# Optimization experiments

Hardware: AMD Instinct MI355X
Metric: run time of the kernel (lower is better)

## Reference

```python
import math
import jax, jax.numpy as jnp
import numpy as np

B, S, H, NH = 4, 2048, 1024, 16
HD = H // NH  # 64


def _rope_cos_sin(seq_len, dim, base=10000.0):
    # freqs[j] = base^(-2j/dim), angles = outer(t, freqs)
    inv = 1.0 / (base ** (jnp.arange(0, dim, 2, dtype=jnp.float32) / dim))
    t = jnp.arange(seq_len, dtype=jnp.float32)
    ang = jnp.outer(t, inv)  # (S, dim//2)
    return jnp.cos(ang), jnp.sin(ang)


def _apply_rope(x, cos, sin):
    # x: (B, S, NH, HD); pairs are (x[2i], x[2i+1]) per torch view_as_complex on reshape(..., -1, 2)
    xr = x.reshape(*x.shape[:-1], HD // 2, 2)
    x0, x1 = xr[..., 0], xr[..., 1]
    c = cos[None, :, None, :]  # (1, S, 1, HD//2)
    s = sin[None, :, None, :]
    o0 = x0 * c - x1 * s
    o1 = x0 * s + x1 * c
    return jnp.stack([o0, o1], axis=-1).reshape(x.shape)


def setup_inputs() -> dict:
    key = jax.random.key(0)
    ks = jax.random.split(key, 5)
    scale = 1.0 / math.sqrt(H)
    return {
        "x": jax.random.normal(ks[0], (B, S, H), dtype=jnp.float32),
        "wq": jax.random.normal(ks[1], (H, H), dtype=jnp.float32) * scale,
        "wk": jax.random.normal(ks[2], (H, H), dtype=jnp.float32) * scale,
        "wv": jax.random.normal(ks[3], (H, H), dtype=jnp.float32) * scale,
        "wo": jax.random.normal(ks[4], (H, H), dtype=jnp.float32) * scale,
        "attention_mask": jnp.ones((B, S), dtype=jnp.int32),
    }


def reference(x, wq, wk, wv, wo, attention_mask):
    # Linear(bias=False): y = x @ W.T with W shape (out, in)
    q = jnp.einsum('bsh,oh->bso', x, wq).reshape(B, S, NH, HD)
    k = jnp.einsum('bsh,oh->bso', x, wk).reshape(B, S, NH, HD)
    v = jnp.einsum('bsh,oh->bso', x, wv).reshape(B, S, NH, HD)
    cos, sin = _rope_cos_sin(S, HD)
    q = _apply_rope(q, cos, sin)
    k = _apply_rope(k, cos, sin)
    # scores: (B, NH, S, S)
    scores = jnp.einsum('bqhd,bkhd->bhqk', q, k) / math.sqrt(HD)
    mask = attention_mask[:, None, None, :]  # (B,1,1,S)
    scores = jnp.where(mask == 0, -jnp.inf, scores)
    attn = jax.nn.softmax(scores, axis=-1)
    # attn_dropout: eval mode / p=0 -> identity
    out = jnp.einsum('bhqk,bkhd->bqhd', attn, v).reshape(B, S, H)
    return jnp.einsum('bsh,oh->bso', out, wo)
```

## Files before the change

### kernel.cpp

```cpp
#include <hip/hip_runtime.h>
#include <hip/hip_bf16.h>

#define B_   4
#define S_   2048
#define H_   1024
#define NH_  16
#define HD_  64
#define M_   8192
#define K_   1024

using bf16x8 = __bf16 __attribute__((ext_vector_type(8)));
using f32x4  = float __attribute__((ext_vector_type(4)));
using f32x16 = float __attribute__((ext_vector_type(16)));

__device__ inline f32x4 mfma16(bf16x8 a, bf16x8 b, f32x4 c) {
    return __builtin_amdgcn_mfma_f32_16x16x32_bf16(a, b, c, 0, 0, 0);
}
__device__ inline f32x16 mfma32(bf16x8 a, bf16x8 b, f32x16 c) {
    return __builtin_amdgcn_mfma_f32_32x32x16_bf16(a, b, c, 0, 0, 0);
}

__device__ inline unsigned short f2bf(float f) {
    __hip_bfloat16 h = __float2bfloat16(f);
    return *reinterpret_cast<unsigned short*>(&h);
}

__device__ inline unsigned cvt_pk_bf16(float lo, float hi) {
    unsigned r;
    asm("v_cvt_pk_bf16_f32 %0, %1, %2" : "=v"(r) : "v"(lo), "v"(hi));
    return r;
}

__device__ inline void perm32swap(unsigned &a, unsigned &b) {
    asm("v_permlane32_swap_b32 %0, %1" : "+v"(a), "+v"(b));
}

__device__ inline void gload_lds16(const unsigned short* g, unsigned short* l) {
    __builtin_amdgcn_global_load_lds(
        (const __attribute__((address_space(1))) void*)g,
        (__attribute__((address_space(3))) void*)l, 16, 0, 0);
}

#define EXP2F(x) __builtin_amdgcn_exp2f(x)


__global__ __launch_bounds__(256) void prep_convert(
    const float* __restrict__ x,  const float* __restrict__ wq,
    const float* __restrict__ wk, const float* __restrict__ wv,
    const float* __restrict__ wo, unsigned short* __restrict__ ws)
{
    size_t u = (size_t)blockIdx.x * 256 + threadIdx.x;
    const float* src; unsigned short* dst; size_t off;
    if (u < 2097152)      { src = x;  dst = ws;            off = u * 4; }
    else if (u < 2359296) { src = wq; dst = ws + 8388608;  off = (u - 2097152) * 4; }
    else if (u < 2621440) { src = wk; dst = ws + 9437184;  off = (u - 2359296) * 4; }
    else if (u < 2883584) { src = wv; dst = ws + 10485760; off = (u - 2621440) * 4; }
    else                  { src = wo; dst = ws + 11534336; off = (u - 2883584) * 4; }
    float4 v = *reinterpret_cast<const float4*>(src + off);
    ushort4 o;
    o.x = f2bf(v.x); o.y = f2bf(v.y); o.z = f2bf(v.z); o.w = f2bf(v.w);
    *reinterpret_cast<ushort4*>(dst + off) = o;
}

__global__ __launch_bounds__(256) void rope_table(
    float2* __restrict__ ropeb, const int* __restrict__ mask,
    float* __restrict__ biasb)
{
    int idx = blockIdx.x * 256 + threadIdx.x;
    int pos = idx >> 5, i = idx & 31;
    float inv = expf(-(float)(2 * i) * (9.210340371976184f / 64.0f));
    float ang = (float)pos * inv;
    float2 cs; cs.x = cosf(ang); cs.y = sinf(ang);
    ropeb[idx] = cs;
    if (idx < B_ * S_)
        biasb[idx] = mask[idx] ? -12.0f : -__builtin_inff();
}

template<int MODE>
__global__ __launch_bounds__(256, 2) void gemm_main(
    const unsigned short* __restrict__ A,
    const unsigned short* __restrict__ W,
    unsigned short* __restrict__ qbuf, unsigned short* __restrict__ kbuf,
    unsigned short* __restrict__ vtb, float* __restrict__ fout,
    const float* __restrict__ ropeb)
{
    __shared__ alignas(16) unsigned short Al[2][128 * 64];
    __shared__ alignas(16) unsigned short Bl[2][128 * 64];

    const int t = threadIdx.x;
    const int l = t & 63;
    const int w = t >> 6;
    const int lane_r = l & 15, lane_g = l >> 4;
    const int bn = blockIdx.x, bm = blockIdx.y;
    const size_t rowbase = (size_t)bm * 128;
    const int colbase = bn * 128;
    const int wm = (w >> 1) * 64, wn = (w & 1) * 64;
    const int which = (MODE == 0) ? (colbase >> 10) : 3;
    const float scale = (which == 0) ? 0.18033688089184827f : 1.0f;

    const int glrow  = l >> 3;
    const int glslot = (l & 7) ^ glrow;
    const unsigned short* ga = A + (rowbase + w * 8 + glrow) * K_ + glslot * 8;
    const unsigned short* gb = W + (size_t)(colbase + w * 8 + glrow) * K_ + glslot * 8;

#define GLA(bi, kt, i) gload_lds16(ga + (size_t)(i) * 32 * K_ + (kt) * 64, \
                                   &Al[bi][((i) * 32 + w * 8) * 64]);
#define GLB(bi, kt, i) gload_lds16(gb + (size_t)(i) * 32 * K_ + (kt) * 64, \
                                   &Bl[bi][((i) * 32 + w * 8) * 64]);
#define RDA(mt, kk) { int rowa = wm + (mt) * 16 + lane_r;                      \
    af[mt][kk] = *reinterpret_cast<const bf16x8*>((const char*)Al[cur] +       \
        ((rowa * 128 + (kk) * 64 + lane_g * 16) ^ ((rowa & 7) << 4))); }
#define RDB(nt, kk) { int rowb = wn + (nt) * 16 + lane_r;                      \
    bfr[nt][kk] = *reinterpret_cast<const bf16x8*>((const char*)Bl[cur] +      \
        ((rowb * 128 + (kk) * 64 + lane_g * 16) ^ ((rowb & 7) << 4))); }
#define MM(mb, nb)                                                             \
    if (MODE == 0 && which <= 1) {                                             \
        _Pragma("unroll")                                                      \
        for (int a = (nb); a < (nb) + 2; a++)                                  \
            _Pragma("unroll")                                                  \
            for (int b2 = (mb); b2 < (mb) + 2; b2++) {                         \
                acc[a][b2] = mfma16(bfr[a][0], af[b2][0], acc[a][b2]);         \
                acc[a][b2] = mfma16(bfr[a][1], af[b2][1], acc[a][b2]);         \
            }                                                                  \
    } else {                                                                   \
        _Pragma("unroll")                                                      \
        for (int mt = (mb); mt < (mb) + 2; mt++)                               \
            _Pragma("unroll")                                                  \
            for (int nt = (nb); nt < (nb) + 2; nt++) {                         \
                acc[mt][nt] = mfma16(af[mt][0], bfr[nt][0], acc[mt][nt]);      \
                acc[mt][nt] = mfma16(af[mt][1], bfr[nt][1], acc[mt][nt]);      \
            }                                                                  \
    }
#define BARS __builtin_amdgcn_s_barrier();                                     \
             asm volatile("s_waitcnt lgkmcnt(0)" ::: "memory");                \
             __builtin_amdgcn_s_setprio(1);
#define BARE __builtin_amdgcn_s_setprio(0); __builtin_amdgcn_s_barrier();

    f32x4 zero4 = {0.f, 0.f, 0.f, 0.f};
    f32x4 acc[4][4];
#pragma unroll
    for (int a = 0; a < 4; a++)
#pragma unroll
        for (int b2 = 0; b2 < 4; b2++) acc[a][b2] = zero4;

    GLA(0, 0, 0) GLA(0, 0, 1) GLA(0, 0, 2) GLA(0, 0, 3)
    GLB(0, 0, 0) GLB(0, 0, 1) GLB(0, 0, 2) GLB(0, 0, 3)
    __syncthreads();

    for (int kt = 0; kt < 16; kt++) {
        const int cur = kt & 1, nxt = cur ^ 1;
        const bool pf = (kt < 15);
        bf16x8 af[4][2], bfr[4][2];
        RDA(0, 0) RDA(0, 1) RDA(1, 0) RDA(1, 1)
        RDB(0, 0) RDB(0, 1) RDB(1, 0) RDB(1, 1)
        if (pf) { GLA(nxt, kt + 1, 0) GLA(nxt, kt + 1, 1) GLA(nxt, kt + 1, 2) }
        BARS MM(0, 0) BARE
        RDB(2, 0) RDB(2, 1) RDB(3, 0) RDB(3, 1)
        if (pf) { GLA(nxt, kt + 1, 3) GLB(nxt, kt + 1, 0) GLB(nxt, kt + 1, 1) }
        BARS MM(0, 2) BARE
        RDA(2, 0) RDA(2, 1) RDA(3, 0) RDA(3, 1)
        if (pf) { GLB(nxt, kt + 1, 2) GLB(nxt, kt + 1, 3) }
        BARS MM(2, 2) BARE
        __builtin_amdgcn_s_setprio(1);
        MM(2, 0)
        __builtin_amdgcn_s_setprio(0);
        asm volatile("s_waitcnt vmcnt(0)" ::: "memory");
        __builtin_amdgcn_s_barrier();
    }
#undef GLA
#undef GLB
#undef RDA
#undef RDB
#undef MM
#undef BARS
#undef BARE

    if (MODE == 1) {
        float* out = fout;
#pragma unroll
        for (int mt = 0; mt < 4; mt++)
#pragma unroll
            for (int nt = 0; nt < 4; nt++)
#pragma unroll
                for (int i = 0; i < 4; i++) {
                    size_t r = rowbase + wm + mt * 16 + lane_g * 4 + i;
                    int n = colbase + wn + nt * 16 + lane_r;
                    out[r * 1024 + n] = acc[mt][nt][i];
                }
    } else if (which <= 1) {
        unsigned short* out = which ? kbuf : qbuf;
#pragma unroll
        for (int a = 0; a < 4; a++) {
            int nbase = (colbase & 1023) + wn + a * 16 + 4 * lane_g;
            int h = nbase >> 6, d0 = nbase & 63;
#pragma unroll
            for (int b2 = 0; b2 < 4; b2++) {
                size_t r = rowbase + wm + b2 * 16 + lane_r;
                int bb  = (int)(r >> 11);
                int pos = (int)(r & 2047);
                float4 cs = *reinterpret_cast<const float4*>(
                    ropeb + pos * 64 + d0);
                float a0 = acc[a][b2][0], a1 = acc[a][b2][1];
                float a2 = acc[a][b2][2], a3 = acc[a][b2][3];
                float o0 = (a0 * cs.x - a1 * cs.y) * scale;
                float o1 = (a0 * cs.y + a1 * cs.x) * scale;
                float o2 = (a2 * cs.z - a3 * cs.w) * scale;
                float o3 = (a2 * cs.w + a3 * cs.z) * scale;
                uint2 o;
                o.x = cvt_pk_bf16(o0, o1);
                o.y = cvt_pk_bf16(o2, o3);
                *reinterpret_cast<uint2*>(
                    out + (((size_t)(bb * NH_ + h)) * S_ + pos) * 64 + d0) = o;
            }
        }
    } else {
#pragma unroll
        for (int a = 0; a < 4; a++)
#pragma unroll
            for (int b2 = 0; b2 < 4; b2++) {
                size_t rr = rowbase + wm + a * 16 + lane_g * 4;
                int n = (colbase & 1023) + wn + b2 * 16 + lane_r;
                int bb  = (int)(rr >> 11);
                int pos = (int)(rr & 2047);
                int h = n >> 6, d = n & 63;
                ushort4 o;
                o.x = f2bf(acc[a][b2][0]); o.y = f2bf(acc[a][b2][1]);
                o.z = f2bf(acc[a][b2][2]); o.w = f2bf(acc[a][b2][3]);
                *reinterpret_cast<ushort4*>(
                    vtb + (((size_t)(bb * NH_ + h)) * 64 + d) * S_ + pos) = o;
            }
    }
}

__global__ __launch_bounds__(256, 2) void attn_fwd(
    const unsigned short* __restrict__ qb, const unsigned short* __restrict__ kb,
    const unsigned short* __restrict__ vt, const float* __restrict__ biasb,
    unsigned short* __restrict__ ao)
{
    __shared__ alignas(16) unsigned short Kl[2][64 * 64];
    __shared__ alignas(16) unsigned short Vl[2][64 * 64];

    const int bid = blockIdx.x;
    const int xcd = bid & 7, idx = bid >> 3;
    const int bh = xcd * 8 + (idx >> 3);
    const int qt = idx & 7;
    const int b = bh >> 4, h = bh & 15;

    const int t = threadIdx.x, l = t & 63, w = t >> 6;
    const int lr = l & 31;
    const int hi = l >> 5;
    const int row8 = lr & 7;

    const unsigned short* qp = qb + (size_t)bh * S_ * 64;
    const unsigned short* kp = kb + (size_t)bh * S_ * 64;
    const unsigned short* vp = vt + (size_t)bh * 64 * S_;
    const float* bp = biasb + (size_t)b * S_;

    bf16x8 qf[2][4];
#pragma unroll
    for (int qbk = 0; qbk < 2; qbk++) {
        int qrow = qt * 256 + w * 64 + qbk * 32 + lr;
#pragma unroll
        for (int ks = 0; ks < 4; ks++)
            qf[qbk][ks] = *reinterpret_cast<const bf16x8*>(
                qp + (size_t)qrow * 64 + ks * 16 + hi * 8);
    }

    f32x16 oacc[2][2];
#pragma unroll
    for (int qbk = 0; qbk < 2; qbk++)
#pragma unroll
        for (int r = 0; r < 16; r++) { oacc[qbk][0][r] = 0.f; oacc[qbk][1][r] = 0.f; }
    float lsum[2] = {0.f, 0.f};

    const int grr = l >> 3;
    const int gss = ((l & 7) ^ grr) * 8;

#define STAGE(bi, kt)                                                          \
    {                                                                          \
        _Pragma("unroll")                                                      \
        for (int c = 0; c < 2; c++) {                                          \
            int rbase = w * 16 + c * 8;                                        \
            gload_lds16(kp + (size_t)((kt) * 64 + rbase + grr) * 64 + gss,     \
                        &Kl[bi][rbase * 64]);                                  \
            gload_lds16(vp + (size_t)(rbase + grr) * S_ + (kt) * 64 + gss,     \
                        &Vl[bi][rbase * 64]);                                  \
        }                                                                      \
    }

    STAGE(0, 0)

    for (int kt = 0; kt < 32; kt++) {
        const int cur = kt & 1;
        __syncthreads();
        if (kt < 31) STAGE(cur ^ 1, kt + 1)

        f32x16 sacc[2][2];
#pragma unroll
        for (int T = 0; T < 2; T++) {
#pragma unroll
            for (int g = 0; g < 4; g++) {
                float4 bv = *reinterpret_cast<const float4*>(
                    bp + kt * 64 + T * 32 + g * 8 + hi * 4);
                sacc[0][T][g * 4 + 0] = bv.x; sacc[0][T][g * 4 + 1] = bv.y;
                sacc[0][T][g * 4 + 2] = bv.z; sacc[0][T][g * 4 + 3] = bv.w;
                sacc[1][T][g * 4 + 0] = bv.x; sacc[1][T][g * 4 + 1] = bv.y;
                sacc[1][T][g * 4 + 2] = bv.z; sacc[1][T][g * 4 + 3] = bv.w;
            }
        }

        __builtin_amdgcn_s_setprio(1);
#pragma unroll
        for (int T = 0; T < 2; T++) {
            int rowb = (32 * T + lr) * 128;
#pragma unroll
            for (int ks = 0; ks < 4; ks++) {
                bf16x8 kf = *reinterpret_cast<const bf16x8*>(
                    (const char*)Kl[cur] + rowb + (((2 * ks + hi) ^ row8) << 4));
                sacc[0][T] = mfma32(kf, qf[0][ks], sacc[0][T]);
                sacc[1][T] = mfma32(kf, qf[1][ks], sacc[1][T]);
            }
        }
        __builtin_amdgcn_s_setprio(0);

        bf16x8 pa[2][4];
#pragma unroll
        for (int qbk = 0; qbk < 2; qbk++) {
            unsigned u[2][8];
            float r0 = 0.f, r1 = 0.f, r2 = 0.f, r3 = 0.f;
#pragma unroll
            for (int T = 0; T < 2; T++) {
                float p[16];
#pragma unroll
                for (int r = 0; r < 16; r++) p[r] = EXP2F(sacc[qbk][T][r]);
#pragma unroll
                for (int r = 0; r < 16; r += 4) {
                    r0 += p[r]; r1 += p[r + 1]; r2 += p[r + 2]; r3 += p[r + 3];
                }
#pragma unroll
                for (int bq = 0; bq < 4; bq++) {
                    u[T][bq * 2 + 0] = cvt_pk_bf16(p[bq * 4 + 0], p[bq * 4 + 1]);
                    u[T][bq * 2 + 1] = cvt_pk_bf16(p[bq * 4 + 2], p[bq * 4 + 3]);
                }
            }
            lsum[qbk] += (r0 + r1) + (r2 + r3);
#pragma unroll
            for (int ks = 0; ks < 4; ks++) {
                int T = ks >> 1, e = ks & 1;
                unsigned a0 = u[T][4 * e + 0], b0 = u[T][4 * e + 2];
                unsigned a1 = u[T][4 * e + 1], b1 = u[T][4 * e + 3];
                perm32swap(a0, b0);
                perm32swap(a1, b1);
                unsigned q4[4] = {a0, a1, b0, b1};
                pa[qbk][ks] = *reinterpret_cast<const bf16x8*>(q4);
            }
        }

        __builtin_amdgcn_s_setprio(1);
#pragma unroll
        for (int dt = 0; dt < 2; dt++) {
            int rowb = (32 * dt + lr) * 128;
#pragma unroll
            for (int ks = 0; ks < 4; ks++) {
                bf16x8 vf = *reinterpret_cast<const bf16x8*>(
                    (const char*)Vl[cur] + rowb + (((2 * ks + hi) ^ row8) << 4));
                oacc[0][dt] = mfma32(vf, pa[0][ks], oacc[0][dt]);
                oacc[1][dt] = mfma32(vf, pa[1][ks], oacc[1][dt]);
            }
        }
        __builtin_amdgcn_s_setprio(0);
    }
#undef STAGE

#pragma unroll
    for (int qbk = 0; qbk < 2; qbk++) {
        float ls = lsum[qbk];
        ls += __shfl_xor(ls, 32);
        float rl = 1.0f / ls;
        size_t obase = ((size_t)(b * S_) + qt * 256 + w * 64 + qbk * 32 + lr) * 1024 + h * 64;
#pragma unroll
        for (int dt = 0; dt < 2; dt++)
#pragma unroll
            for (int g = 0; g < 4; g++) {
                uint2 o;
                o.x = cvt_pk_bf16(oacc[qbk][dt][g * 4 + 0] * rl, oacc[qbk][dt][g * 4 + 1] * rl);
                o.y = cvt_pk_bf16(oacc[qbk][dt][g * 4 + 2] * rl, oacc[qbk][dt][g * 4 + 3] * rl);
                *reinterpret_cast<uint2*>(ao + obase + 32 * dt + 8 * g + 4 * hi) = o;
            }
    }
}

extern "C" void kernel_launch(void* const* d_in, const int* in_sizes, int n_in,
                              void* d_out, int out_size, void* d_ws, size_t ws_size,
                              hipStream_t stream)
{
    const float* x  = (const float*)d_in[0];
    const float* wq = (const float*)d_in[1];
    const float* wk = (const float*)d_in[2];
    const float* wv = (const float*)d_in[3];
    const float* wo = (const float*)d_in[4];
    const int* mask = (const int*)d_in[5];

    unsigned short* ws   = (unsigned short*)d_ws;
    unsigned short* xb   = ws;
    unsigned short* wqkv = ws + 8388608;
    unsigned short* wob  = ws + 11534336;
    unsigned short* qbuf = ws + 12582912;
    unsigned short* kbuf = ws + 20971520;
    unsigned short* vtb  = ws + 29360128;
    float* ropeb = (float*)(ws + 37748736);
    float* biasb = (float*)(ws + 38010880);
    unsigned short* aob = xb;

    prep_convert<<<12288, 256, 0, stream>>>(x, wq, wk, wv, wo, ws);
    rope_table<<<256, 256, 0, stream>>>((float2*)ropeb, mask, biasb);

    gemm_main<0><<<dim3(24, 64), 256, 0, stream>>>(
        xb, wqkv, qbuf, kbuf, vtb, nullptr, ropeb);

    attn_fwd<<<512, 256, 0, stream>>>(qbuf, kbuf, vtb, biasb, aob);

    gemm_main<1><<<dim3(8, 64), 256, 0, stream>>>(
        aob, wob, nullptr, nullptr, nullptr, (float*)d_out, nullptr);
}
```

Measured before the change: 199.4 us.

## Use 256x256 tiles with 8 waves for fused QKV projection GEMM

Replaces the shared 128x128 GEMM template for the QKV projection with a dedicated kernel using 256x256 block tiles, 512 threads (8 waves, each computing 128x64), and a two-deep LDS pipeline that prefetches tile kt+2 while computing kt. The output projection becomes a separate simplified kernel. The goal is to raise arithmetic intensity and cut global/LDS reload traffic per MFMA. The cost is 128KB of LDS per block and 128 accumulator registers per thread, which lowers occupancy. The grid also shrinks to 384 blocks, which may underfill the CUs.

```diff
diff --git a/kernel.cpp b/kernel.cpp
--- a/kernel.cpp
+++ b/kernel.cpp
@@ -39,6 +39,11 @@
     __builtin_amdgcn_global_load_lds(
         (const __attribute__((address_space(1))) void*)g,
         (__attribute__((address_space(3))) void*)l, 16, 0, 0);
+}
+
+__device__ inline bf16x8 ldfrag(const unsigned short* base, int row, int kk, int lane_g) {
+    int off = (row * 128 + kk * 64 + lane_g * 16) ^ ((row & 7) << 4);
+    return *reinterpret_cast<const bf16x8*>((const char*)base + off);
 }
 
 #define EXP2F(x) __builtin_amdgcn_exp2f(x)
@@ -76,13 +81,177 @@
         biasb[idx] = mask[idx] ? -12.0f : -__builtin_inff();
 }
 
-template<int MODE>
-__global__ __launch_bounds__(256, 2) void gemm_main(
+__global__ __launch_bounds__(512, 2) void gemm_qkv256(
     const unsigned short* __restrict__ A,
     const unsigned short* __restrict__ W,
     unsigned short* __restrict__ qbuf, unsigned short* __restrict__ kbuf,
-    unsigned short* __restrict__ vtb, float* __restrict__ fout,
+    unsigned short* __restrict__ vtb,
     const float* __restrict__ ropeb)
+{
+    __shared__ alignas(16) unsigned short Al[2][256 * 64];
+    __shared__ alignas(16) unsigned short Bl[2][256 * 64];
+
+    const int t = threadIdx.x;
+    const int l = t & 63;
+    const int w = t >> 6;
+    const int lane_r = l & 15, lane_g = l >> 4;
+    const int bn = blockIdx.x, bm = blockIdx.y;
+    const size_t rowbase = (size_t)bm * 256;
+    const int colbase = bn * 256;
+    const int wr = w >> 2, wc = w & 3;
+    const int wm = wr * 128, wn = wc * 64;
+    const int which = bn >> 2;
+    const float scale = (which == 0) ? 0.18033688089184827f : 1.0f;
+
+    const int grr = l >> 3;
+    const int gss = ((l & 7) ^ grr) * 8;
+    const unsigned short* ga = A + (rowbase + w * 8 + grr) * K_ + gss;
+    const unsigned short* gb = W + (size_t)(colbase + w * 8 + grr) * K_ + gss;
+
+#define STAGE(bi, kt)                                                          \
+    { _Pragma("unroll")                                                        \
+      for (int c = 0; c < 4; c++) {                                            \
+          gload_lds16(ga + (size_t)(c * 64) * K_ + (kt) * 64,                  \
+                      &Al[bi][(c * 64 + w * 8) * 64]);                         \
+          gload_lds16(gb + (size_t)(c * 64) * K_ + (kt) * 64,                  \
+                      &Bl[bi][(c * 64 + w * 8) * 64]);                         \
+      } }
+
+#define BARF asm volatile("" ::: "memory");                                    \
+             __builtin_amdgcn_s_barrier();                                     \
+             asm volatile("" ::: "memory");
+#define PRIO1 __builtin_amdgcn_s_setprio(1);
+#define PRIO0 __builtin_amdgcn_s_setprio(0);
+
+#define QMM(MT0, NT0)                                                          \
+    if (which <= 1) {                                                          \
+        _Pragma("unroll")                                                      \
+        for (int mt = (MT0); mt < (MT0) + 4; mt++)                             \
+            _Pragma("unroll")                                                  \
+            for (int nt = (NT0); nt < (NT0) + 2; nt++) {                       \
+                acc[mt][nt] = mfma16(bfr[nt][0], af[mt - (MT0)][0], acc[mt][nt]); \
+                acc[mt][nt] = mfma16(bfr[nt][1], af[mt - (MT0)][1], acc[mt][nt]); \
+            }                                                                  \
+    } else {                                                                   \
+        _Pragma("unroll")                                                      \
+        for (int mt = (MT0); mt < (MT0) + 4; mt++)                             \
+            _Pragma("unroll")                                                  \
+            for (int nt = (NT0); nt < (NT0) + 2; nt++) {                       \
+                acc[mt][nt] = mfma16(af[mt - (MT0)][0], bfr[nt][0], acc[mt][nt]); \
+                acc[mt][nt] = mfma16(af[mt - (MT0)][1], bfr[nt][1], acc[mt][nt]); \
+            }                                                                  \
+    }
+
+#define TILE_PHASES(cur, kt, DO_ISSUE)                                         \
+    {                                                                          \
+        bf16x8 af[4][2], bfr[4][2];                                            \
+            \
+        _Pragma("unroll")                                                      \
+        for (int i = 0; i < 4; i++) {                                          \
+            int rowa = wm + i * 16 + lane_r;                                   \
+            af[i][0] = ldfrag(Al[cur], rowa, 0, lane_g);                       \
+            af[i][1] = ldfrag(Al[cur], rowa, 1, lane_g);                       \
+        }                                                                      \
+        _Pragma("unroll")                                                      \
+        for (int nt = 0; nt < 2; nt++) {                                       \
+            int rowb = wn + nt * 16 + lane_r;                                  \
+            bfr[nt][0] = ldfrag(Bl[cur], rowb, 0, lane_g);                     \
+            bfr[nt][1] = ldfrag(Bl[cur], rowb, 1, lane_g);                     \
+        }                                                                      \
+        BARF PRIO1 QMM(0, 0) PRIO0 BARF                                        \
+                              \
+        _Pragma("unroll")                                                      \
+        for (int nt = 2; nt < 4; nt++) {                                       \
+            int rowb = wn + nt * 16 + lane_r;                                  \
+            bfr[nt][0] = ldfrag(Bl[cur], rowb, 0, lane_g);                     \
+            bfr[nt][1] = ldfrag(Bl[cur], rowb, 1, lane_g);                     \
+        }                                                                      \
+        BARF PRIO1 QMM(0, 2) PRIO0 BARF                                        \
+             \
+        _Pragma("unroll")                                                      \
+        for (int i = 0; i < 4; i++) {                                          \
+            int rowa = wm + (i + 4) * 16 + lane_r;                             \
+            af[i][0] = ldfrag(Al[cur], rowa, 0, lane_g);                       \
+            af[i][1] = ldfrag(Al[cur], rowa, 1, lane_g);                       \
+        }                                                                      \
+        BARF PRIO1 QMM(4, 2) PRIO0 BARF                                        \
+            \
+        if (DO_ISSUE) STAGE(cur, (kt) + 2)                                     \
+        BARF PRIO1 QMM(4, 0) PRIO0                                             \
+        if (DO_ISSUE) { asm volatile("s_waitcnt vmcnt(8)" ::: "memory"); }     \
+        else          { asm volatile("s_waitcnt vmcnt(0)" ::: "memory"); }     \
+        BARF                                                                   \
+    }
+
+    f32x4 zero4 = {0.f, 0.f, 0.f, 0.f};
+    f32x4 acc[8][4];
+#pragma unroll
+    for (int a = 0; a < 8; a++)
+#pragma unroll
+        for (int b2 = 0; b2 < 4; b2++) acc[a][b2] = zero4;
+
+    STAGE(0, 0) STAGE(1, 1)
+    asm volatile("s_waitcnt vmcnt(8)" ::: "memory");
+    __builtin_amdgcn_s_barrier();
+
+    for (int it = 0; it < 8; it++) {
+        const bool pf = (it < 7);
+        TILE_PHASES(0, 2 * it, pf)
+        TILE_PHASES(1, 2 * it + 1, pf)
+    }
+#undef STAGE
+#undef QMM
+#undef TILE_PHASES
+
+    if (which <= 1) {
+        unsigned short* out = which ? kbuf : qbuf;
+#pragma unroll
+        for (int nt = 0; nt < 4; nt++) {
+            int nfull = (colbase & 1023) + wn + nt * 16 + 4 * lane_g;
+            int h = nfull >> 6, d0 = nfull & 63;
+#pragma unroll
+            for (int mt = 0; mt < 8; mt++) {
+                size_t r = rowbase + wm + mt * 16 + lane_r;
+                int bb  = (int)(r >> 11);
+                int pos = (int)(r & 2047);
+                float4 cs = *reinterpret_cast<const float4*>(
+                    ropeb + pos * 64 + d0);
+                float a0 = acc[mt][nt][0], a1 = acc[mt][nt][1];
+                float a2 = acc[mt][nt][2], a3 = acc[mt][nt][3];
+                float o0 = (a0 * cs.x - a1 * cs.y) * scale;
+                float o1 = (a0 * cs.y + a1 * cs.x) * scale;
+                float o2 = (a2 * cs.z - a3 * cs.w) * scale;
+                float o3 = (a2 * cs.w + a3 * cs.z) * scale;
+                uint2 o;
+                o.x = cvt_pk_bf16(o0, o1);
+                o.y = cvt_pk_bf16(o2, o3);
+                *reinterpret_cast<uint2*>(
+                    out + (((size_t)(bb * NH_ + h)) * S_ + pos) * 64 + d0) = o;
+            }
+        }
+    } else {
+#pragma unroll
+        for (int mt = 0; mt < 8; mt++)
+#pragma unroll
+            for (int nt = 0; nt < 4; nt++) {
+                size_t rr = rowbase + wm + mt * 16 + lane_g * 4;
+                int n = (colbase & 1023) + wn + nt * 16 + lane_r;
+                int bb  = (int)(rr >> 11);
+                int pos = (int)(rr & 2047);
+                int h = n >> 6, d = n & 63;
+                ushort4 o;
+                o.x = f2bf(acc[mt][nt][0]); o.y = f2bf(acc[mt][nt][1]);
+                o.z = f2bf(acc[mt][nt][2]); o.w = f2bf(acc[mt][nt][3]);
+                *reinterpret_cast<ushort4*>(
+                    vtb + (((size_t)(bb * NH_ + h)) * 64 + d) * S_ + pos) = o;
+            }
+    }
+}
+
+__global__ __launch_bounds__(256, 2) void gemm_wo(
+    const unsigned short* __restrict__ A,
+    const unsigned short* __restrict__ W,
+    float* __restrict__ fout)
 {
     __shared__ alignas(16) unsigned short Al[2][128 * 64];
     __shared__ alignas(16) unsigned short Bl[2][128 * 64];
@@ -95,8 +264,6 @@
     const size_t rowbase = (size_t)bm * 128;
     const int colbase = bn * 128;
     const int wm = (w >> 1) * 64, wn = (w & 1) * 64;
-    const int which = (MODE == 0) ? (colbase >> 10) : 3;
-    const float scale = (which == 0) ? 0.18033688089184827f : 1.0f;
 
     const int glrow  = l >> 3;
     const int glslot = (l & 7) ^ glrow;
@@ -114,23 +281,13 @@
     bfr[nt][kk] = *reinterpret_cast<const bf16x8*>((const char*)Bl[cur] +      \
         ((rowb * 128 + (kk) * 64 + lane_g * 16) ^ ((rowb & 7) << 4))); }
 #define MM(mb, nb)                                                             \
-    if (MODE == 0 && which <= 1) {                                             \
-        _Pragma("unroll")                                                      \
-        for (int a = (nb); a < (nb) + 2; a++)                                  \
-            _Pragma("unroll")                                                  \
-            for (int b2 = (mb); b2 < (mb) + 2; b2++) {                         \
-                acc[a][b2] = mfma16(bfr[a][0], af[b2][0], acc[a][b2]);         \
-                acc[a][b2] = mfma16(bfr[a][1], af[b2][1], acc[a][b2]);         \
-            }                                                                  \
-    } else {                                                                   \
-        _Pragma("unroll")                                                      \
-        for (int mt = (mb); mt < (mb) + 2; mt++)                               \
-            _Pragma("unroll")                                                  \
-            for (int nt = (nb); nt < (nb) + 2; nt++) {                         \
-                acc[mt][nt] = mfma16(af[mt][0], bfr[nt][0], acc[mt][nt]);      \
-                acc[mt][nt] = mfma16(af[mt][1], bfr[nt][1], acc[mt][nt]);      \
-            }                                                                  \
-    }
+    { _Pragma("unroll")                                                        \
+      for (int mt = (mb); mt < (mb) + 2; mt++)                                 \
+          _Pragma("unroll")                                                    \
+          for (int nt = (nb); nt < (nb) + 2; nt++) {                           \
+              acc[mt][nt] = mfma16(af[mt][0], bfr[nt][0], acc[mt][nt]);        \
+              acc[mt][nt] = mfma16(af[mt][1], bfr[nt][1], acc[mt][nt]);        \
+          } }
 #define BARS __builtin_amdgcn_s_barrier();                                     \
              asm volatile("s_waitcnt lgkmcnt(0)" ::: "memory");                \
              __builtin_amdgcn_s_setprio(1);
@@ -175,61 +332,16 @@
 #undef BARS
 #undef BARE
 
-    if (MODE == 1) {
-        float* out = fout;
-#pragma unroll
-        for (int mt = 0; mt < 4; mt++)
-#pragma unroll
-            for (int nt = 0; nt < 4; nt++)
-#pragma unroll
-                for (int i = 0; i < 4; i++) {
-                    size_t r = rowbase + wm + mt * 16 + lane_g * 4 + i;
-                    int n = colbase + wn + nt * 16 + lane_r;
-                    out[r * 1024 + n] = acc[mt][nt][i];
-                }
-    } else if (which <= 1) {
-        unsigned short* out = which ? kbuf : qbuf;
-#pragma unroll
-        for (int a = 0; a < 4; a++) {
-            int nbase = (colbase & 1023) + wn + a * 16 + 4 * lane_g;
-            int h = nbase >> 6, d0 = nbase & 63;
-#pragma unroll
-            for (int b2 = 0; b2 < 4; b2++) {
-                size_t r = rowbase + wm + b2 * 16 + lane_r;
-                int bb  = (int)(r >> 11);
-                int pos = (int)(r & 2047);
-                float4 cs = *reinterpret_cast<const float4*>(
-                    ropeb + pos * 64 + d0);
-                float a0 = acc[a][b2][0], a1 = acc[a][b2][1];
-                float a2 = acc[a][b2][2], a3 = acc[a][b2][3];
-                float o0 = (a0 * cs.x - a1 * cs.y) * scale;
-                float o1 = (a0 * cs.y + a1 * cs.x) * scale;
-                float o2 = (a2 * cs.z - a3 * cs.w) * scale;
-                float o3 = (a2 * cs.w + a3 * cs.z) * scale;
-                uint2 o;
-                o.x = cvt_pk_bf16(o0, o1);
-                o.y = cvt_pk_bf16(o2, o3);
-                *reinterpret_cast<uint2*>(
-                    out + (((size_t)(bb * NH_ + h)) * S_ + pos) * 64 + d0) = o;
-            }
-        }
-    } else {
-#pragma unroll
-        for (int a = 0; a < 4; a++)
-#pragma unroll
-            for (int b2 = 0; b2 < 4; b2++) {
-                size_t rr = rowbase + wm + a * 16 + lane_g * 4;
-                int n = (colbase & 1023) + wn + b2 * 16 + lane_r;
-                int bb  = (int)(rr >> 11);
-                int pos = (int)(rr & 2047);
-                int h = n >> 6, d = n & 63;
-                ushort4 o;
-                o.x = f2bf(acc[a][b2][0]); o.y = f2bf(acc[a][b2][1]);
-                o.z = f2bf(acc[a][b2][2]); o.w = f2bf(acc[a][b2][3]);
-                *reinterpret_cast<ushort4*>(
-                    vtb + (((size_t)(bb * NH_ + h)) * 64 + d) * S_ + pos) = o;
-            }
-    }
+#pragma unroll
+    for (int mt = 0; mt < 4; mt++)
+#pragma unroll
+        for (int nt = 0; nt < 4; nt++)
+#pragma unroll
+            for (int i = 0; i < 4; i++) {
+                size_t r = rowbase + wm + mt * 16 + lane_g * 4 + i;
+                int n = colbase + wn + nt * 16 + lane_r;
+                fout[r * 1024 + n] = acc[mt][nt][i];
+            }
 }
 
 __global__ __launch_bounds__(256, 2) void attn_fwd(
@@ -415,11 +527,9 @@
     prep_convert<<<12288, 256, 0, stream>>>(x, wq, wk, wv, wo, ws);
     rope_table<<<256, 256, 0, stream>>>((float2*)ropeb, mask, biasb);
 
-    gemm_main<0><<<dim3(24, 64), 256, 0, stream>>>(
-        xb, wqkv, qbuf, kbuf, vtb, nullptr, ropeb);
+    gemm_qkv256<<<dim3(12, 32), 512, 0, stream>>>(xb, wqkv, qbuf, kbuf, vtb, ropeb);
 
     attn_fwd<<<512, 256, 0, stream>>>(qbuf, kbuf, vtb, biasb, aob);
 
-    gemm_main<1><<<dim3(8, 64), 256, 0, stream>>>(
-        aob, wob, nullptr, nullptr, nullptr, (float*)d_out, nullptr);
-}
+    gemm_wo<<<dim3(8, 64), 256, 0, stream>>>(aob, wob, (float*)d_out);
+}
```

New measurement: 391.8 us. 1.97x slower.
